# Optimization experiments

Hardware: AMD Instinct MI355X
Metric: run time of the kernel (lower is better)

Reference implementation:

```python
import jax, jax.numpy as jnp
import numpy as np

D_MODEL = 1024
N_HEAD = 16
DH = D_MODEL // N_HEAD


def setup_inputs() -> dict:
    key = jax.random.key(0)
    ks = jax.random.split(key, 5)
    B, T = 4, 2048
    scale = 0.02
    return {
        "x": jax.random.normal(ks[0], (B, T, D_MODEL), dtype=jnp.float32),
        "Wqkv": jax.random.normal(ks[1], (D_MODEL, 3 * D_MODEL), dtype=jnp.float32) * scale,
        "bqkv": jnp.zeros((3 * D_MODEL,), dtype=jnp.float32),
        "Wout": jax.random.normal(ks[2], (D_MODEL, D_MODEL), dtype=jnp.float32) * scale,
        "bout": jnp.zeros((D_MODEL,), dtype=jnp.float32),
    }


def reference(x, Wqkv, bqkv, Wout, bout):
    B, T, C = x.shape
    qkv = x @ Wqkv + bqkv  # [B,T,3C]
    q, k, v = jnp.split(qkv, 3, axis=2)
    # [B,T,C] -> [B,H,T,dh]
    def heads(t):
        return t.reshape(B, T, N_HEAD, DH).transpose(0, 2, 1, 3)
    q, k, v = heads(q), heads(k), heads(v)
    scores = jnp.einsum("bhqd,bhkd->bhqk", q, k) / jnp.sqrt(jnp.float32(DH))
    causal = jnp.tril(jnp.ones((T, T), dtype=bool))  # [T,T]
    neg = jnp.finfo(scores.dtype).min
    scores = jnp.where(causal[None, None, :, :], scores, neg)
    A = jax.nn.softmax(scores, axis=-1)
    y = jnp.einsum("bhqk,bhkd->bhqd", A, v)
    y = y.transpose(0, 2, 1, 3).reshape(B, T, C)
    return y @ Wout + bout
```

## Files before the change

kernel.cpp:

```cpp
#include <hip/hip_runtime.h>
#include <hip/hip_bf16.h>

typedef float f32x4 __attribute__((ext_vector_type(4)));
typedef short s16x8 __attribute__((ext_vector_type(8)));
typedef short s16x4 __attribute__((ext_vector_type(4)));
typedef unsigned int u32x4 __attribute__((ext_vector_type(4)));

#define B_ 4
#define T_ 2048
#define C_ 1024
#define H_ 16
#define DH_ 64
#define M_ (B_*T_)
#define N3_ (3*C_)

static __device__ __forceinline__ short f2bf(float f) {
    __hip_bfloat16 h = __float2bfloat16(f);
    return *reinterpret_cast<short*>(&h);
}

static __device__ __forceinline__ unsigned pack2(float lo, float hi) {
    unsigned lb = (unsigned short)f2bf(lo);
    unsigned hb = (unsigned short)f2bf(hi);
    return lb | (hb << 16);
}

static __device__ __forceinline__ void gload16(const void* g, void* l) {
    __builtin_amdgcn_global_load_lds(
        (const __attribute__((address_space(1))) void*)g,
        (__attribute__((address_space(3))) void*)l, 16, 0, 0);
}

static __device__ __forceinline__ s16x8 lds_frag(const short* base, int row, int chunk) {
    return *(const s16x8*)&base[(row << 6) + ((chunk ^ (row & 7)) << 3)];
}


__global__ __launch_bounds__(256) void cast_f32_bf16(
    const float* __restrict__ in, short* __restrict__ out, int n8)
{
    int i = blockIdx.x * 256 + threadIdx.x;
    if (i >= n8) return;
    float4 a = *(const float4*)&in[i * 8];
    float4 b = *(const float4*)&in[i * 8 + 4];
    s16x8 o = { f2bf(a.x), f2bf(a.y), f2bf(a.z), f2bf(a.w),
                f2bf(b.x), f2bf(b.y), f2bf(b.z), f2bf(b.w) };
    *(s16x8*)&out[i * 8] = o;
}

__global__ __launch_bounds__(256) void transpose_cast(
    const float* __restrict__ src, short* __restrict__ dst, int K, int N)
{
    __shared__ short t[64][66];
    int tid = threadIdx.x;
    int n0 = blockIdx.x * 64, k0 = blockIdx.y * 64;
    #pragma unroll
    for (int p = 0; p < 4; ++p) {
        int cid = tid + p * 256;
        int r = cid >> 4, c4 = cid & 15;
        float4 v = *(const float4*)&src[(size_t)(k0 + r) * N + n0 + c4 * 4];
        t[r][c4 * 4 + 0] = f2bf(v.x);
        t[r][c4 * 4 + 1] = f2bf(v.y);
        t[r][c4 * 4 + 2] = f2bf(v.z);
        t[r][c4 * 4 + 3] = f2bf(v.w);
    }
    __syncthreads();
    #pragma unroll
    for (int p = 0; p < 4; ++p) {
        int cid = tid + p * 256;
        int r = cid >> 4, c4 = cid & 15;
        s16x4 ov;
        #pragma unroll
        for (int j = 0; j < 4; ++j) ov[j] = t[c4 * 4 + j][r];
        *(s16x4*)&dst[(size_t)(n0 + r) * K + k0 + c4 * 4] = ov;
    }
}


template<int MODE>
__global__ __launch_bounds__(256) void gemm_bt(
    const short* __restrict__ A, const short* __restrict__ Bt,
    const float* __restrict__ bias, float* __restrict__ out,
    short* __restrict__ qout, short* __restrict__ kout, short* __restrict__ vout)
{
    const int K = 1024;
    __shared__ short As[128 * 64];
    __shared__ short Bs[128 * 64];
    int tid = threadIdx.x;
    int lane = tid & 63, w = tid >> 6;
    int d = lane & 15, g = lane >> 4;
    int wm = w >> 1, wn = w & 1;
    int m0 = blockIdx.y * 128, n0 = blockIdx.x * 128;

    f32x4 acc[4][4];
    #pragma unroll
    for (int i = 0; i < 4; ++i)
        #pragma unroll
        for (int j = 0; j < 4; ++j) acc[i][j] = (f32x4){0.f, 0.f, 0.f, 0.f};

    for (int kt = 0; kt < K; kt += 64) {
        #pragma unroll
        for (int p = 0; p < 4; ++p) {
            int cid = p * 256 + tid;
            int r = cid >> 3, c8 = cid & 7;
            int co = (c8 ^ (r & 7)) << 3;
            int dofs = (p * 256 + (tid & ~63)) * 8;
            gload16(&A[(size_t)(m0 + r) * K + kt + co], &As[dofs]);
            gload16(&Bt[(size_t)(n0 + r) * K + kt + co], &Bs[dofs]);
        }
        __syncthreads();
        #pragma unroll
        for (int ks = 0; ks < 2; ++ks) {
            s16x8 af[4], bf[4];
            #pragma unroll
            for (int i = 0; i < 4; ++i) {
                af[i] = lds_frag(As, wm * 64 + i * 16 + d, ks * 4 + g);
                bf[i] = lds_frag(Bs, wn * 64 + i * 16 + d, ks * 4 + g);
            }
            #pragma unroll
            for (int mi = 0; mi < 4; ++mi)
                #pragma unroll
                for (int ni = 0; ni < 4; ++ni)
                    acc[mi][ni] = __builtin_amdgcn_mfma_f32_16x16x32_bf16(
                        af[mi], bf[ni], acc[mi][ni], 0, 0, 0);
        }
        __syncthreads();
    }

    #pragma unroll
    for (int mi = 0; mi < 4; ++mi)
        #pragma unroll
        for (int ni = 0; ni < 4; ++ni) {
            int gn = n0 + wn * 64 + ni * 16 + d;
            float bv = bias[gn];
            int gm0 = m0 + wm * 64 + mi * 16 + g * 4;
            if (MODE == 0) {
                #pragma unroll
                for (int r = 0; r < 4; ++r)
                    out[(size_t)(gm0 + r) * 1024 + gn] = acc[mi][ni][r] + bv;
            } else {
                int which = gn >> 10, cc = gn & 1023;
                int h = cc >> 6, dh = cc & 63;
                int b = gm0 >> 11, t0 = gm0 & 2047;
                if (which == 2) {
                    s16x4 pv;
                    #pragma unroll
                    for (int r = 0; r < 4; ++r) pv[r] = f2bf(acc[mi][ni][r] + bv);
                    *(s16x4*)&vout[((size_t)(b * 16 + h) * 64 + dh) * 2048 + t0] = pv;
                } else if (which == 1) {
                    #pragma unroll
                    for (int r = 0; r < 4; ++r)
                        kout[((size_t)(b * 16 + h) * 2048 + (t0 + r)) * 64 + dh] =
                            f2bf(acc[mi][ni][r] + bv);
                } else {
                    const float SC2 = 0.125f * 1.44269504089f;
                    #pragma unroll
                    for (int r = 0; r < 4; ++r)
                        qout[((size_t)(b * 16 + h) * 2048 + (t0 + r)) * 64 + dh] =
                            f2bf((acc[mi][ni][r] + bv) * SC2);
                }
            }
        }
}


__global__ __launch_bounds__(256, 4) void attn_fwd(
    const short* __restrict__ q, const short* __restrict__ kk,
    const short* __restrict__ vt, short* __restrict__ y)
{
    __shared__ short Ks[2][64 * 64];
    __shared__ short Vs[2][64 * 64];
    int tid = threadIdx.x, lane = tid & 63, w = tid >> 6;
    int d = lane & 15, g = lane >> 4;
    int bid = blockIdx.x;
    int bh = (bid & 7) | ((bid >> 7) << 3);
    int pi = (bid >> 3) & 15;
    int b = bh >> 4, h = bh & 15;
    const size_t hb = (size_t)bh * 2048 * 64;

    const bool isg0 = (g == 0), isg3 = (g == 3);
    const bool up = lane >= 32;

    #define STAGE(buf, kt2) do { \
        _Pragma("unroll") \
        for (int p = 0; p < 2; ++p) { \
            int cid = p * 256 + tid; \
            int r__ = cid >> 3, c8__ = cid & 7; \
            int co__ = (c8__ ^ (r__ & 7)) << 3; \
            int dofs__ = (p * 256 + (tid & ~63)) * 8; \
            gload16(&kk[hb + (size_t)((kt2) * 64 + r__) * 64 + co__], &Ks[buf][dofs__]); \
            gload16(&vt[hb + (size_t)r__ * 2048 + (kt2) * 64 + co__], &Vs[buf][dofs__]); \
        } \
    } while (0)

    #pragma unroll 1
    for (int pass = 0; pass < 2; ++pass) {
        int qt = pass ? (31 - pi) : pi;
        int nt = qt + 1;
        int qrow = qt * 64 + w * 16;
        int qg = qrow + d;

        s16x8 qf0 = *(const s16x8*)&q[hb + (size_t)(qrow + d) * 64 + 8 * g];
        s16x8 qf1 = *(const s16x8*)&q[hb + (size_t)(qrow + d) * 64 + 32 + 8 * g];

        f32x4 o[4];
        float l = 0.f;
        #pragma unroll
        for (int r = 0; r < 4; ++r) o[r] = (f32x4){0.f, 0.f, 0.f, 0.f};

        STAGE(0, 0);
        int cur = 0;

        #pragma unroll 1
        for (int t = 0; t < nt; ++t) {
            if (t + 1 < nt) {
                STAGE(cur ^ 1, t + 1);
                asm volatile("s_waitcnt vmcnt(4)" ::: "memory");
            } else {
                asm volatile("s_waitcnt vmcnt(0)" ::: "memory");
            }
            __builtin_amdgcn_s_barrier();

            if (t * 64 <= qrow + 15) {
                const short* Kb = Ks[cur];
                const short* Vb = Vs[cur];

                f32x4 s[4];
                #pragma unroll
                for (int ni = 0; ni < 4; ++ni) {
                    s[ni] = (f32x4){0.f, 0.f, 0.f, 0.f};
                    s[ni] = __builtin_amdgcn_mfma_f32_16x16x32_bf16(
                        lds_frag(Kb, ni * 16 + d, g), qf0, s[ni], 0, 0, 0);
                    s[ni] = __builtin_amdgcn_mfma_f32_16x16x32_bf16(
                        lds_frag(Kb, ni * 16 + d, 4 + g), qf1, s[ni], 0, 0, 0);
                }

                float pv[4][4];
                if (t * 64 + 63 > qrow) {
                    #pragma unroll
                    for (int ni = 0; ni < 4; ++ni)
                        #pragma unroll
                        for (int r = 0; r < 4; ++r) {
                            int kg = t * 64 + ni * 16 + g * 4 + r;
                            pv[ni][r] = (kg > qg) ? 0.f : exp2f(s[ni][r]);
                        }
                } else {
                    #pragma unroll
                    for (int ni = 0; ni < 4; ++ni)
                        #pragma unroll
                        for (int r = 0; r < 4; ++r)
                            pv[ni][r] = exp2f(s[ni][r]);
                }

                float S = ((pv[0][0] + pv[0][1]) + (pv[0][2] + pv[0][3]))
                        + ((pv[1][0] + pv[1][1]) + (pv[1][2] + pv[1][3]))
                        + ((pv[2][0] + pv[2][1]) + (pv[2][2] + pv[2][3]))
                        + ((pv[3][0] + pv[3][1]) + (pv[3][2] + pv[3][3]));
                S += __shfl_xor(S, 16);
                S += __shfl_xor(S, 32);
                l += S;

                unsigned W[4][2], X[4][2];
                #pragma unroll
                for (int ni = 0; ni < 4; ++ni)
                    #pragma unroll
                    for (int rp = 0; rp < 2; ++rp)
                        W[ni][rp] = pack2(pv[ni][2 * rp], pv[ni][2 * rp + 1]);
                #pragma unroll
                for (int ni = 0; ni < 4; ++ni)
                    #pragma unroll
                    for (int rp = 0; rp < 2; ++rp)
                        X[ni][rp] = __shfl_xor((int)W[ni][rp], 16);

                unsigned P0 = up ? X[0][0] : W[1][0];
                unsigned P1 = up ? X[0][1] : W[1][1];
                unsigned P2 = up ? W[0][0] : X[1][0];
                unsigned P3 = up ? W[0][1] : X[1][1];
                unsigned P4 = up ? X[2][0] : W[3][0];
                unsigned P5 = up ? X[2][1] : W[3][1];
                unsigned P6 = up ? W[2][0] : X[3][0];
                unsigned P7 = up ? W[2][1] : X[3][1];
                unsigned R0 = __shfl_xor((int)P0, 32);
                unsigned R1 = __shfl_xor((int)P1, 32);
                unsigned R2 = __shfl_xor((int)P2, 32);
                unsigned R3 = __shfl_xor((int)P3, 32);
                unsigned R4 = __shfl_xor((int)P4, 32);
                unsigned R5 = __shfl_xor((int)P5, 32);
                unsigned R6 = __shfl_xor((int)P6, 32);
                unsigned R7 = __shfl_xor((int)P7, 32);

                unsigned F0 = isg0 ? W[0][0] : isg3 ? X[1][0] : R0;
                unsigned F1 = isg0 ? W[0][1] : isg3 ? X[1][1] : R1;
                unsigned F2 = isg0 ? X[0][0] : isg3 ? W[1][0] : R2;
                unsigned F3 = isg0 ? X[0][1] : isg3 ? W[1][1] : R3;
                unsigned F4 = isg0 ? W[2][0] : isg3 ? X[3][0] : R4;
                unsigned F5 = isg0 ? W[2][1] : isg3 ? X[3][1] : R5;
                unsigned F6 = isg0 ? X[2][0] : isg3 ? W[3][0] : R6;
                unsigned F7 = isg0 ? X[2][1] : isg3 ? W[3][1] : R7;

                u32x4 w0 = {F0, F1, F2, F3};
                u32x4 w1 = {F4, F5, F6, F7};
                s16x8 pa0 = __builtin_bit_cast(s16x8, w0);
                s16x8 pa1 = __builtin_bit_cast(s16x8, w1);

                #pragma unroll
                for (int df = 0; df < 4; ++df) {
                    o[df] = __builtin_amdgcn_mfma_f32_16x16x32_bf16(
                        pa0, lds_frag(Vb, df * 16 + d, g), o[df], 0, 0, 0);
                    o[df] = __builtin_amdgcn_mfma_f32_16x16x32_bf16(
                        pa1, lds_frag(Vb, df * 16 + d, 4 + g), o[df], 0, 0, 0);
                }
            }

            __builtin_amdgcn_s_barrier();
            cur ^= 1;
        }

        #pragma unroll
        for (int r = 0; r < 4; ++r) {
            float lr = __shfl(l, g * 4 + r);
            float rl = 1.0f / lr;
            int grow = qrow + g * 4 + r;
            #pragma unroll
            for (int df = 0; df < 4; ++df)
                y[(size_t)(b * 2048 + grow) * 1024 + h * 64 + df * 16 + d] =
                    f2bf(o[df][r] * rl);
        }
    }
    #undef STAGE
}


extern "C" void kernel_launch(void* const* d_in, const int* in_sizes, int n_in,
                              void* d_out, int out_size, void* d_ws, size_t ws_size,
                              hipStream_t stream)
{
    const float* x    = (const float*)d_in[0];
    const float* Wqkv = (const float*)d_in[1];
    const float* bqkv = (const float*)d_in[2];
    const float* Wout = (const float*)d_in[3];
    const float* bout = (const float*)d_in[4];
    float* out = (float*)d_out;

    char* ws = (char*)d_ws;
    short* xbf   = (short*)ws;  ws += (size_t)M_ * C_ * 2;
    short* wqkvT = (short*)ws;  ws += (size_t)N3_ * C_ * 2;
    short* woutT = (short*)ws;  ws += (size_t)C_ * C_ * 2;
    short* qb    = (short*)ws;  ws += (size_t)M_ * C_ * 2;
    short* kb    = (short*)ws;  ws += (size_t)M_ * C_ * 2;
    short* vtb   = (short*)ws;  ws += (size_t)M_ * C_ * 2;
    short* yb    = (short*)ws;  ws += (size_t)M_ * C_ * 2;

    cast_f32_bf16<<<(M_ * C_ / 8 + 255) / 256, 256, 0, stream>>>(x, xbf, M_ * C_ / 8);
    transpose_cast<<<dim3(N3_ / 64, C_ / 64), 256, 0, stream>>>(Wqkv, wqkvT, C_, N3_);
    transpose_cast<<<dim3(C_ / 64, C_ / 64), 256, 0, stream>>>(Wout, woutT, C_, C_);

    gemm_bt<1><<<dim3(N3_ / 128, M_ / 128), 256, 0, stream>>>(
        xbf, wqkvT, bqkv, nullptr, qb, kb, vtb);

    attn_fwd<<<dim3((T_ / 64 / 2) * B_ * H_), 256, 0, stream>>>(qb, kb, vtb, yb);

    gemm_bt<0><<<dim3(C_ / 128, M_ / 128), 256, 0, stream>>>(
        yb, woutT, bout, out, nullptr, nullptr, nullptr);
}
```

Measured before the change: 197.6 us.

## Rewrite attention with 32x32 MFMA tiles and 128-row query blocks

The attention kernel switches from 16x16x32 to 32x32x16 bf16 MFMA, so each wave handles 32 query rows and each block covers a 128-row query tile. Before, blocks paired a short and a long query tile to balance causal work. Now each block does one tile, scheduled longest first. The new output layout lets P feed the PV MFMA directly, which removes the cross-lane shuffle shuffling of P and the per-tile row-sum reductions, and output stores are vectorized. In exchange, the larger accumulators raise register pressure and the causal load balance now depends on launch order.

```diff
diff --git a/kernel.cpp b/kernel.cpp
--- a/kernel.cpp
+++ b/kernel.cpp
@@ -2,6 +2,7 @@
 #include <hip/hip_bf16.h>
 
 typedef float f32x4 __attribute__((ext_vector_type(4)));
+typedef float f32x16 __attribute__((ext_vector_type(16)));
 typedef short s16x8 __attribute__((ext_vector_type(8)));
 typedef short s16x4 __attribute__((ext_vector_type(4)));
 typedef unsigned int u32x4 __attribute__((ext_vector_type(4)));
@@ -33,6 +34,13 @@
 
 static __device__ __forceinline__ s16x8 lds_frag(const short* base, int row, int chunk) {
     return *(const s16x8*)&base[(row << 6) + ((chunk ^ (row & 7)) << 3)];
+}
+
+static __device__ __forceinline__ s16x8 vfrag(const short* base, int row, int kc, int h) {
+    int r7 = row & 7;
+    s16x4 a = *(const s16x4*)&base[(row << 6) + (((2 * kc) ^ r7) << 3) + 4 * h];
+    s16x4 b = *(const s16x4*)&base[(row << 6) + (((2 * kc + 1) ^ r7) << 3) + 4 * h];
+    return __builtin_shufflevector(a, b, 0, 1, 2, 3, 4, 5, 6, 7);
 }
 
 
@@ -170,16 +178,28 @@
 {
     __shared__ short Ks[2][64 * 64];
     __shared__ short Vs[2][64 * 64];
-    int tid = threadIdx.x, lane = tid & 63, w = tid >> 6;
-    int d = lane & 15, g = lane >> 4;
+    int tid = threadIdx.x, w = tid >> 6;
+    int lane = tid & 63;
+    int q5 = lane & 31, h5 = lane >> 5;
     int bid = blockIdx.x;
-    int bh = (bid & 7) | ((bid >> 7) << 3);
-    int pi = (bid >> 3) & 15;
-    int b = bh >> 4, h = bh & 15;
+    int idx = bid >> 3;
+    int qt = 15 - (idx >> 3);
+    int bh = ((idx & 7) << 3) | (bid & 7);
+    int b = bh >> 4, hh = bh & 15;
     const size_t hb = (size_t)bh * 2048 * 64;
-
-    const bool isg0 = (g == 0), isg3 = (g == 3);
-    const bool up = lane >= 32;
+    int nt = 2 * qt + 2;
+    int qrow = qt * 128 + w * 32;
+    int qg = qrow + q5;
+
+    s16x8 qf[4];
+    #pragma unroll
+    for (int s = 0; s < 4; ++s)
+        qf[s] = *(const s16x8*)&q[hb + (size_t)qg * 64 + 16 * s + 8 * h5];
+
+    f32x16 oA, oB;
+    #pragma unroll
+    for (int i = 0; i < 16; ++i) { oA[i] = 0.f; oB[i] = 0.f; }
+    float l = 0.f;
 
     #define STAGE(buf, kt2) do { \
         _Pragma("unroll") \
@@ -193,139 +213,101 @@
         } \
     } while (0)
 
+    STAGE(0, 0);
+    int cur = 0;
+
     #pragma unroll 1
-    for (int pass = 0; pass < 2; ++pass) {
-        int qt = pass ? (31 - pi) : pi;
-        int nt = qt + 1;
-        int qrow = qt * 64 + w * 16;
-        int qg = qrow + d;
-
-        s16x8 qf0 = *(const s16x8*)&q[hb + (size_t)(qrow + d) * 64 + 8 * g];
-        s16x8 qf1 = *(const s16x8*)&q[hb + (size_t)(qrow + d) * 64 + 32 + 8 * g];
-
-        f32x4 o[4];
-        float l = 0.f;
-        #pragma unroll
-        for (int r = 0; r < 4; ++r) o[r] = (f32x4){0.f, 0.f, 0.f, 0.f};
-
-        STAGE(0, 0);
-        int cur = 0;
-
-        #pragma unroll 1
-        for (int t = 0; t < nt; ++t) {
-            if (t + 1 < nt) {
-                STAGE(cur ^ 1, t + 1);
-                asm volatile("s_waitcnt vmcnt(4)" ::: "memory");
+    for (int t = 0; t < nt; ++t) {
+        if (t + 1 < nt) {
+            STAGE(cur ^ 1, t + 1);
+            asm volatile("s_waitcnt vmcnt(4)" ::: "memory");
+        } else {
+            asm volatile("s_waitcnt vmcnt(0)" ::: "memory");
+        }
+        __builtin_amdgcn_s_barrier();
+
+        if (t * 64 <= qrow + 31) {
+            const short* Kb = Ks[cur];
+            const short* Vb = Vs[cur];
+
+            f32x16 sA, sB;
+            #pragma unroll
+            for (int i = 0; i < 16; ++i) { sA[i] = 0.f; sB[i] = 0.f; }
+            #pragma unroll
+            for (int s = 0; s < 4; ++s) {
+                sA = __builtin_amdgcn_mfma_f32_32x32x16_bf16(
+                    lds_frag(Kb, q5, 2 * s + h5), qf[s], sA, 0, 0, 0);
+                sB = __builtin_amdgcn_mfma_f32_32x32x16_bf16(
+                    lds_frag(Kb, 32 + q5, 2 * s + h5), qf[s], sB, 0, 0, 0);
+            }
+
+            float eA[16], eB[16];
+            float S = 0.f;
+            if (t * 64 + 63 > qrow) {
+                #pragma unroll
+                for (int rg = 0; rg < 16; ++rg) {
+                    int kg = t * 64 + (rg & 3) + 8 * (rg >> 2) + 4 * h5;
+                    float a = exp2f(sA[rg]); if (kg > qg) a = 0.f;
+                    float c = exp2f(sB[rg]); if (kg + 32 > qg) c = 0.f;
+                    eA[rg] = a; eB[rg] = c; S += a + c;
+                }
             } else {
-                asm volatile("s_waitcnt vmcnt(0)" ::: "memory");
-            }
-            __builtin_amdgcn_s_barrier();
-
-            if (t * 64 <= qrow + 15) {
-                const short* Kb = Ks[cur];
-                const short* Vb = Vs[cur];
-
-                f32x4 s[4];
                 #pragma unroll
-                for (int ni = 0; ni < 4; ++ni) {
-                    s[ni] = (f32x4){0.f, 0.f, 0.f, 0.f};
-                    s[ni] = __builtin_amdgcn_mfma_f32_16x16x32_bf16(
-                        lds_frag(Kb, ni * 16 + d, g), qf0, s[ni], 0, 0, 0);
-                    s[ni] = __builtin_amdgcn_mfma_f32_16x16x32_bf16(
-                        lds_frag(Kb, ni * 16 + d, 4 + g), qf1, s[ni], 0, 0, 0);
+                for (int rg = 0; rg < 16; ++rg) {
+                    float a = exp2f(sA[rg]);
+                    float c = exp2f(sB[rg]);
+                    eA[rg] = a; eB[rg] = c; S += a + c;
                 }
-
-                float pv[4][4];
-                if (t * 64 + 63 > qrow) {
-                    #pragma unroll
-                    for (int ni = 0; ni < 4; ++ni)
-                        #pragma unroll
-                        for (int r = 0; r < 4; ++r) {
-                            int kg = t * 64 + ni * 16 + g * 4 + r;
-                            pv[ni][r] = (kg > qg) ? 0.f : exp2f(s[ni][r]);
-                        }
-                } else {
-                    #pragma unroll
-                    for (int ni = 0; ni < 4; ++ni)
-                        #pragma unroll
-                        for (int r = 0; r < 4; ++r)
-                            pv[ni][r] = exp2f(s[ni][r]);
-                }
-
-                float S = ((pv[0][0] + pv[0][1]) + (pv[0][2] + pv[0][3]))
-                        + ((pv[1][0] + pv[1][1]) + (pv[1][2] + pv[1][3]))
-                        + ((pv[2][0] + pv[2][1]) + (pv[2][2] + pv[2][3]))
-                        + ((pv[3][0] + pv[3][1]) + (pv[3][2] + pv[3][3]));
-                S += __shfl_xor(S, 16);
-                S += __shfl_xor(S, 32);
-                l += S;
-
-                unsigned W[4][2], X[4][2];
-                #pragma unroll
-                for (int ni = 0; ni < 4; ++ni)
-                    #pragma unroll
-                    for (int rp = 0; rp < 2; ++rp)
-                        W[ni][rp] = pack2(pv[ni][2 * rp], pv[ni][2 * rp + 1]);
-                #pragma unroll
-                for (int ni = 0; ni < 4; ++ni)
-                    #pragma unroll
-                    for (int rp = 0; rp < 2; ++rp)
-                        X[ni][rp] = __shfl_xor((int)W[ni][rp], 16);
-
-                unsigned P0 = up ? X[0][0] : W[1][0];
-                unsigned P1 = up ? X[0][1] : W[1][1];
-                unsigned P2 = up ? W[0][0] : X[1][0];
-                unsigned P3 = up ? W[0][1] : X[1][1];
-                unsigned P4 = up ? X[2][0] : W[3][0];
-                unsigned P5 = up ? X[2][1] : W[3][1];
-                unsigned P6 = up ? W[2][0] : X[3][0];
-                unsigned P7 = up ? W[2][1] : X[3][1];
-                unsigned R0 = __shfl_xor((int)P0, 32);
-                unsigned R1 = __shfl_xor((int)P1, 32);
-                unsigned R2 = __shfl_xor((int)P2, 32);
-                unsigned R3 = __shfl_xor((int)P3, 32);
-                unsigned R4 = __shfl_xor((int)P4, 32);
-                unsigned R5 = __shfl_xor((int)P5, 32);
-                unsigned R6 = __shfl_xor((int)P6, 32);
-                unsigned R7 = __shfl_xor((int)P7, 32);
-
-                unsigned F0 = isg0 ? W[0][0] : isg3 ? X[1][0] : R0;
-                unsigned F1 = isg0 ? W[0][1] : isg3 ? X[1][1] : R1;
-                unsigned F2 = isg0 ? X[0][0] : isg3 ? W[1][0] : R2;
-                unsigned F3 = isg0 ? X[0][1] : isg3 ? W[1][1] : R3;
-                unsigned F4 = isg0 ? W[2][0] : isg3 ? X[3][0] : R4;
-                unsigned F5 = isg0 ? W[2][1] : isg3 ? X[3][1] : R5;
-                unsigned F6 = isg0 ? X[2][0] : isg3 ? W[3][0] : R6;
-                unsigned F7 = isg0 ? X[2][1] : isg3 ? W[3][1] : R7;
-
-                u32x4 w0 = {F0, F1, F2, F3};
-                u32x4 w1 = {F4, F5, F6, F7};
-                s16x8 pa0 = __builtin_bit_cast(s16x8, w0);
-                s16x8 pa1 = __builtin_bit_cast(s16x8, w1);
-
-                #pragma unroll
-                for (int df = 0; df < 4; ++df) {
-                    o[df] = __builtin_amdgcn_mfma_f32_16x16x32_bf16(
-                        pa0, lds_frag(Vb, df * 16 + d, g), o[df], 0, 0, 0);
-                    o[df] = __builtin_amdgcn_mfma_f32_16x16x32_bf16(
-                        pa1, lds_frag(Vb, df * 16 + d, 4 + g), o[df], 0, 0, 0);
-                }
-            }
-
-            __builtin_amdgcn_s_barrier();
-            cur ^= 1;
-        }
-
-        #pragma unroll
-        for (int r = 0; r < 4; ++r) {
-            float lr = __shfl(l, g * 4 + r);
-            float rl = 1.0f / lr;
-            int grow = qrow + g * 4 + r;
-            #pragma unroll
-            for (int df = 0; df < 4; ++df)
-                y[(size_t)(b * 2048 + grow) * 1024 + h * 64 + df * 16 + d] =
-                    f2bf(o[df][r] * rl);
-        }
+            }
+            l += S;
+
+            unsigned wdA[8], wdB[8];
+            #pragma unroll
+            for (int m = 0; m < 4; ++m) {
+                wdA[2 * m]     = pack2(eA[4 * m],     eA[4 * m + 1]);
+                wdA[2 * m + 1] = pack2(eA[4 * m + 2], eA[4 * m + 3]);
+                wdB[2 * m]     = pack2(eB[4 * m],     eB[4 * m + 1]);
+                wdB[2 * m + 1] = pack2(eB[4 * m + 2], eB[4 * m + 3]);
+            }
+
+            #pragma unroll
+            for (int kc = 0; kc < 2; ++kc) {
+                u32x4 pw = {wdA[4 * kc], wdA[4 * kc + 1], wdA[4 * kc + 2], wdA[4 * kc + 3]};
+                s16x8 pb = __builtin_bit_cast(s16x8, pw);
+                oA = __builtin_amdgcn_mfma_f32_32x32x16_bf16(
+                    vfrag(Vb, q5, kc, h5), pb, oA, 0, 0, 0);
+                oB = __builtin_amdgcn_mfma_f32_32x32x16_bf16(
+                    vfrag(Vb, 32 + q5, kc, h5), pb, oB, 0, 0, 0);
+            }
+            #pragma unroll
+            for (int kc = 0; kc < 2; ++kc) {
+                u32x4 pw = {wdB[4 * kc], wdB[4 * kc + 1], wdB[4 * kc + 2], wdB[4 * kc + 3]};
+                s16x8 pb = __builtin_bit_cast(s16x8, pw);
+                oA = __builtin_amdgcn_mfma_f32_32x32x16_bf16(
+                    vfrag(Vb, q5, kc + 2, h5), pb, oA, 0, 0, 0);
+                oB = __builtin_amdgcn_mfma_f32_32x32x16_bf16(
+                    vfrag(Vb, 32 + q5, kc + 2, h5), pb, oB, 0, 0, 0);
+            }
+        }
+
+        __builtin_amdgcn_s_barrier();
+        cur ^= 1;
+    }
+
+    l += __shfl_xor(l, 32);
+    float rl = 1.0f / l;
+
+    short* yp = &y[(size_t)(b * 2048 + qg) * 1024 + hh * 64];
+    #pragma unroll
+    for (int m = 0; m < 4; ++m) {
+        s16x4 v0, v1;
+        #pragma unroll
+        for (int i = 0; i < 4; ++i) {
+            v0[i] = f2bf(oA[4 * m + i] * rl);
+            v1[i] = f2bf(oB[4 * m + i] * rl);
+        }
+        *(s16x4*)&yp[8 * m + 4 * h5] = v0;
+        *(s16x4*)&yp[32 + 8 * m + 4 * h5] = v1;
     }
     #undef STAGE
 }
@@ -358,7 +340,7 @@
     gemm_bt<1><<<dim3(N3_ / 128, M_ / 128), 256, 0, stream>>>(
         xbf, wqkvT, bqkv, nullptr, qb, kb, vtb);
 
-    attn_fwd<<<dim3((T_ / 64 / 2) * B_ * H_), 256, 0, stream>>>(qb, kb, vtb, yb);
+    attn_fwd<<<dim3((T_ / 128) * B_ * H_), 256, 0, stream>>>(qb, kb, vtb, yb);
 
     gemm_bt<0><<<dim3(C_ / 128, M_ / 128), 256, 0, stream>>>(
         yb, woutT, bout, out, nullptr, nullptr, nullptr);
```

Result: faster. 185.9 us (-5.9%).
